# Kernel tuning notes

Measured on AMD Instinct MI355X. Metric: run time of the kernel, lower is better.

The kernel has to match this reference:

```python
import jax, jax.numpy as jnp
import numpy as np

N, E, H, C, NG = 50000, 800000, 4, 64, 32
HC = H * C  # 256


def setup_inputs() -> dict:
    key = jax.random.key(0)
    ks = jax.random.split(key, 32)
    f32 = jnp.float32
    def rn(k, shape, s=0.1):
        return jax.random.normal(k, shape, dtype=f32) * s
    inp = {}
    inp['x'] = jax.random.normal(ks[0], (N, 4), dtype=f32)
    inp['edge_index'] = jax.random.randint(ks[1], (2, E), 0, N, dtype=jnp.int32)
    inp['edge_attr'] = jax.random.normal(ks[2], (E, 1), dtype=f32)
    inp['batch'] = jnp.sort(jax.random.randint(ks[3], (N,), 0, NG, dtype=jnp.int32))
    # encoder
    inp['enc_w'] = rn(ks[4], (4, 64)); inp['enc_b'] = rn(ks[5], (64,))
    # GATv2 layer 1: in 64 -> H*C (lin_l source, lin_r target, lin_edge, att, bias)
    inp['g1_wl'] = rn(ks[6], (64, HC)); inp['g1_bl'] = rn(ks[7], (HC,))
    inp['g1_wr'] = rn(ks[8], (64, HC)); inp['g1_br'] = rn(ks[9], (HC,))
    inp['g1_we'] = rn(ks[10], (1, HC))
    inp['g1_att'] = rn(ks[11], (H, C))
    inp['g1_bias'] = rn(ks[12], (HC,))
    # GATv2 layer 2: in 256 -> H*C
    inp['g2_wl'] = rn(ks[13], (HC, HC)); inp['g2_bl'] = rn(ks[14], (HC,))
    inp['g2_wr'] = rn(ks[15], (HC, HC)); inp['g2_br'] = rn(ks[16], (HC,))
    inp['g2_we'] = rn(ks[17], (1, HC))
    inp['g2_att'] = rn(ks[18], (H, C))
    inp['g2_bias'] = rn(ks[19], (HC,))
    # post MLP: 256 -> 128 (LayerNorm, ReLU) -> 64 (ReLU)
    inp['p1_w'] = rn(ks[20], (HC, 128)); inp['p1_b'] = rn(ks[21], (128,))
    inp['ln_g'] = jnp.ones((128,), dtype=f32); inp['ln_b'] = jnp.zeros((128,), dtype=f32)
    inp['p2_w'] = rn(ks[22], (128, 64)); inp['p2_b'] = rn(ks[23], (64,))
    return inp


def _gatv2_layer(x, src, dst, eattr, wl, bl, wr, br, we, att, bias):
    # PyG GATv2Conv: alpha_e = att . leaky_relu(lin_l(x_src) + lin_r(x_dst) + lin_edge(e))
    n = x.shape[0]
    xl = (x @ wl + bl).reshape(n, H, C)   # source-side messages
    xr = (x @ wr + br).reshape(n, H, C)   # target-side
    e = (eattr @ we).reshape(-1, H, C)
    m = jax.nn.leaky_relu(xl[src] + xr[dst] + e, 0.2)        # [E',H,C]
    alpha = jnp.einsum('ehc,hc->eh', m, att)                  # [E',H]
    amax = jax.lax.stop_gradient(jax.ops.segment_max(alpha, dst, num_segments=n))
    ex = jnp.exp(alpha - amax[dst])
    den = jax.ops.segment_sum(ex, dst, num_segments=n)
    a = ex / den[dst]                                          # softmax per dst node
    out = jax.ops.segment_sum(a[:, :, None] * xl[src], dst, num_segments=n)
    return out.reshape(n, HC) + bias


def reference(x, edge_index, edge_attr, batch, enc_w, enc_b,
              g1_wl, g1_bl, g1_wr, g1_br, g1_we, g1_att, g1_bias,
              g2_wl, g2_bl, g2_wr, g2_br, g2_we, g2_att, g2_bias,
              p1_w, p1_b, ln_g, ln_b, p2_w, p2_b):
    n = x.shape[0]
    src0, dst0 = edge_index[0], edge_index[1]
    # PyG default add_self_loops=True with fill_value='mean' for edge_attr
    deg = jnp.maximum(jax.ops.segment_sum(jnp.ones_like(edge_attr[:, 0]), dst0, num_segments=n), 1.0)
    loop_attr = jax.ops.segment_sum(edge_attr, dst0, num_segments=n) / deg[:, None]
    idx = jnp.arange(n, dtype=src0.dtype)
    src = jnp.concatenate([src0, idx]); dst = jnp.concatenate([dst0, idx])
    eattr = jnp.concatenate([edge_attr, loop_attr], axis=0)
    h = jax.nn.relu(x @ enc_w + enc_b)
    h = jax.nn.relu(_gatv2_layer(h, src, dst, eattr, g1_wl, g1_bl, g1_wr, g1_br, g1_we, g1_att, g1_bias))
    h = jax.nn.relu(_gatv2_layer(h, src, dst, eattr, g2_wl, g2_bl, g2_wr, g2_br, g2_we, g2_att, g2_bias))
    # global mean pool over graphs
    cnt = jnp.maximum(jax.ops.segment_sum(jnp.ones((n,), h.dtype), batch, num_segments=NG), 1.0)
    g = jax.ops.segment_sum(h, batch, num_segments=NG) / cnt[:, None]
    # post MLP (dropout is identity in eval)
    z = g @ p1_w + p1_b
    mu = jnp.mean(z, axis=-1, keepdims=True)
    var = jnp.mean((z - mu) ** 2, axis=-1, keepdims=True)
    z = (z - mu) / jnp.sqrt(var + 1e-5) * ln_g + ln_b
    z = jax.nn.relu(z)
    z = jax.nn.relu(z @ p2_w + p2_b)
    return z
```

## Files before the change

kernel.cpp:

```cpp
#include <hip/hip_runtime.h>

#define CDIV(a,b) (((a)+(b)-1)/(b))

typedef __bf16 bf16_t;
typedef bf16_t bf16x8 __attribute__((ext_vector_type(8)));
typedef bf16_t bf16x4 __attribute__((ext_vector_type(4)));
typedef float floatx4 __attribute__((ext_vector_type(4)));
typedef float floatx2 __attribute__((ext_vector_type(2)));

__device__ __forceinline__ int sigma2(int p) {
    int tile = p >> 7, hh = (p >> 6) & 1, m = (p >> 2) & 15, c = p & 3;
    return tile * 128 + (hh * 4 + c) * 16 + m;
}

__device__ __forceinline__ floatx2 up2(unsigned v) {
    floatx2 r;
    r.x = __uint_as_float(v << 16);
    r.y = __uint_as_float(v & 0xffff0000u);
    return r;
}

__global__ void k_deg(const int* __restrict__ ei, const float* __restrict__ ea,
                      int* __restrict__ deg, float* __restrict__ lsum, int E) {
    int e = blockIdx.x * 256 + threadIdx.x;
    if (e >= E) return;
    int d = ei[E + e];
    atomicAdd(&deg[d], 1);
    atomicAdd(&lsum[d], ea[e]);
}

__global__ void k_scanA(const int* __restrict__ deg, int* __restrict__ part, int n) {
    __shared__ int sh[256];
    int t = threadIdx.x;
    int i = blockIdx.x * 256 + t;
    int v = (i < n) ? deg[i] + 1 : 0;
    sh[t] = v;
    __syncthreads();
    for (int d = 128; d > 0; d >>= 1) { if (t < d) sh[t] += sh[t + d]; __syncthreads(); }
    if (t == 0) part[blockIdx.x] = sh[0];
}
__global__ void k_scanB(int* __restrict__ part, int nb) {
    __shared__ int sh[256];
    int t = threadIdx.x;
    int v = (t < nb) ? part[t] : 0;
    sh[t] = v;
    __syncthreads();
    for (int d = 1; d < 256; d <<= 1) {
        int u = (t >= d) ? sh[t - d] : 0;
        __syncthreads();
        sh[t] += u;
        __syncthreads();
    }
    if (t < nb) part[t] = sh[t] - v;
}
__global__ void k_scanC(const int* __restrict__ deg, const int* __restrict__ part,
                        int* __restrict__ off, float* __restrict__ lsum, int n) {
    __shared__ int sh[256];
    int t = threadIdx.x;
    int i = blockIdx.x * 256 + t;
    int dv = (i < n) ? deg[i] : 0;
    int v = (i < n) ? dv + 1 : 0;
    sh[t] = v;
    __syncthreads();
    for (int d = 1; d < 256; d <<= 1) {
        int u = (t >= d) ? sh[t - d] : 0;
        __syncthreads();
        sh[t] += u;
        __syncthreads();
    }
    int excl = part[blockIdx.x] + sh[t] - v;
    if (i < n) {
        off[i] = excl;
        lsum[i] = lsum[i] / fmaxf((float)dv, 1.0f);
    }
    if (i == n - 1) off[n] = excl + v;
}

__global__ void k_fill(const int* __restrict__ ei, const float* __restrict__ ea,
                       const float* __restrict__ lattr, const int* __restrict__ off,
                       int* __restrict__ cursor, int2* __restrict__ csr, int E, int n) {
    int e = blockIdx.x * 256 + threadIdx.x;
    int EE = E + n;
    if (e >= EE) return;
    int s, d; float a;
    if (e < E) { s = ei[e]; d = ei[E + e]; a = ea[e]; }
    else       { s = e - E; d = s;         a = lattr[s]; }
    int pos = off[d] + atomicAdd(&cursor[d], 1);
    csr[pos] = make_int2(s, __float_as_int(a));
}

__global__ void k_wcast2(const float* __restrict__ Wl, const float* __restrict__ Wr,
                         const float* __restrict__ bl, const float* __restrict__ br,
                         bf16_t* __restrict__ Wt, float* __restrict__ bias2,
                         int K, int kshift, int permK,
                         const float* __restrict__ we, const float* __restrict__ att,
                         const float* __restrict__ cb,
                         float* __restrict__ wep, float* __restrict__ attp,
                         float* __restrict__ cbp) {
    int idx = blockIdx.x * 256 + threadIdx.x;
    if (idx < 512) bias2[idx] = (idx < 256) ? bl[idx] : br[idx - 256];
    if (idx < 256) {
        int sg = sigma2(idx);
        wep[idx] = we[sg]; attp[idx] = att[sg]; cbp[idx] = cb[sg];
    }
    if (idx >= 512 * K) return;
    int nn = idx >> kshift, k = idx & (K - 1);
    int ks = permK ? sigma2(k) : k;
    float v = (nn < 256) ? Wl[ks * 256 + nn] : Wr[ks * 256 + (nn - 256)];
    Wt[idx] = (bf16_t)v;
}

__global__ __launch_bounds__(256) void k_gemm1_fused(
        const float* __restrict__ x, const float* __restrict__ encw,
        const float* __restrict__ encb, const bf16_t* __restrict__ Wt,
        const float* __restrict__ bias2, bf16_t* __restrict__ XL,
        bf16_t* __restrict__ XR, int nrows) {
    __shared__ bf16_t As[128 * 32];
    __shared__ bf16_t Bs[128 * 32];
    int tid = threadIdx.x;
    int w = tid >> 6, lane = tid & 63;
    int quad = lane >> 4, m = lane & 15;
    int row0 = blockIdx.x * 128;
    bf16x8 afr[2][2];
    floatx4 acc[2][8];

    for (int ctile = 0; ctile < 4; ++ctile) {
        int n0 = ctile * 128;
#pragma unroll
        for (int rt = 0; rt < 2; ++rt)
#pragma unroll
            for (int ct = 0; ct < 8; ++ct)
                acc[rt][ct] = (floatx4){0.f, 0.f, 0.f, 0.f};
        for (int k0c = 0; k0c < 2; ++k0c) {
            __syncthreads();
            if (ctile == 0) {
#pragma unroll
                for (int i = 0; i < 2; ++i) {
                    int c = tid + i * 256;
                    int r = c >> 2, kc = c & 3;
                    int sw = (kc + (r >> 1)) & 3;
                    int gr = row0 + r; if (gr >= nrows) gr = nrows - 1;
                    float4 xv = ((const float4*)x)[gr];
                    bf16x8 v;
#pragma unroll
                    for (int kk = 0; kk < 8; ++kk) {
                        int k = k0c * 32 + kc * 8 + kk;
                        float s = encb[k];
                        s = fmaf(xv.x, encw[k], s);
                        s = fmaf(xv.y, encw[64 + k], s);
                        s = fmaf(xv.z, encw[128 + k], s);
                        s = fmaf(xv.w, encw[192 + k], s);
                        v[kk] = (bf16_t)fmaxf(s, 0.0f);
                    }
                    *(bf16x8*)&As[r * 32 + sw * 8] = v;
                }
            }
#pragma unroll
            for (int i = 0; i < 2; ++i) {
                int c = tid + i * 256;
                int r = c >> 2, kc = c & 3;
                int sw = (kc + (r >> 1)) & 3;
                bf16x8 v = *(const bf16x8*)&Wt[(size_t)(n0 + r) * 64 + k0c * 32 + kc * 8];
                *(bf16x8*)&Bs[r * 32 + sw * 8] = v;
            }
            __syncthreads();
            if (ctile == 0) {
#pragma unroll
                for (int rt = 0; rt < 2; ++rt) {
                    int ar = w * 32 + rt * 16 + m;
                    afr[k0c][rt] = *(bf16x8*)&As[ar * 32 + (((quad + (ar >> 1)) & 3) * 8)];
                }
            }
            bf16x8 bfr[8];
#pragma unroll
            for (int ct = 0; ct < 8; ++ct) {
                int br = ct * 16 + m;
                bfr[ct] = *(bf16x8*)&Bs[br * 32 + (((quad + (br >> 1)) & 3) * 8)];
            }
#pragma unroll
            for (int ct = 0; ct < 8; ++ct) {
                acc[0][ct] = __builtin_amdgcn_mfma_f32_16x16x32_bf16(afr[k0c][0], bfr[ct], acc[0][ct], 0, 0, 0);
                acc[1][ct] = __builtin_amdgcn_mfma_f32_16x16x32_bf16(afr[k0c][1], bfr[ct], acc[1][ct], 0, 0, 0);
            }
        }
        int tile = ctile & 1;
        bf16_t* dst = (ctile < 2) ? XL : XR;
        float bv[8];
#pragma unroll
        for (int ct = 0; ct < 8; ++ct) bv[ct] = bias2[n0 + ct * 16 + m];
#pragma unroll
        for (int rt = 0; rt < 2; ++rt) {
#pragma unroll
            for (int i = 0; i < 4; ++i) {
                int row = row0 + w * 32 + rt * 16 + quad * 4 + i;
                if (row < nrows) {
                    bf16x4 v0, v1;
#pragma unroll
                    for (int ct = 0; ct < 4; ++ct) {
                        v0[ct] = (bf16_t)(acc[rt][ct][i] + bv[ct]);
                        v1[ct] = (bf16_t)(acc[rt][ct + 4][i] + bv[ct + 4]);
                    }
                    *(bf16x4*)&dst[(size_t)row * 256 + tile * 128 + m * 4] = v0;
                    *(bf16x4*)&dst[(size_t)row * 256 + tile * 128 + 64 + m * 4] = v1;
                }
            }
        }
    }
}

__global__ __launch_bounds__(256) void k_gemm2(
        const bf16_t* __restrict__ Hb, const bf16_t* __restrict__ Wt,
        const float* __restrict__ bias2, bf16_t* __restrict__ XL,
        bf16_t* __restrict__ XR, int nrows) {
    const int K = 256;
    __shared__ bf16_t As[128 * 32];
    __shared__ bf16_t Bs[128 * 32];
    int tid = threadIdx.x;
    int w = tid >> 6, lane = tid & 63;
    int quad = lane >> 4, m = lane & 15;
    int row0 = blockIdx.x * 128;
    bf16x8 afr[8][2];
    floatx4 acc[2][8];

    for (int ctile = 0; ctile < 4; ++ctile) {
        int n0 = ctile * 128;
#pragma unroll
        for (int rt = 0; rt < 2; ++rt)
#pragma unroll
            for (int ct = 0; ct < 8; ++ct)
                acc[rt][ct] = (floatx4){0.f, 0.f, 0.f, 0.f};
        for (int k0c = 0; k0c < 8; ++k0c) {
            __syncthreads();
            if (ctile == 0) {
#pragma unroll
                for (int i = 0; i < 2; ++i) {
                    int c = tid + i * 256;
                    int r = c >> 2, kc = c & 3;
                    int sw = (kc + (r >> 1)) & 3;
                    int gr = row0 + r; if (gr >= nrows) gr = nrows - 1;
                    bf16x8 v = *(const bf16x8*)&Hb[(size_t)gr * K + k0c * 32 + kc * 8];
                    *(bf16x8*)&As[r * 32 + sw * 8] = v;
                }
            }
#pragma unroll
            for (int i = 0; i < 2; ++i) {
                int c = tid + i * 256;
                int r = c >> 2, kc = c & 3;
                int sw = (kc + (r >> 1)) & 3;
                bf16x8 v = *(const bf16x8*)&Wt[(size_t)(n0 + r) * K + k0c * 32 + kc * 8];
                *(bf16x8*)&Bs[r * 32 + sw * 8] = v;
            }
            __syncthreads();
            if (ctile == 0) {
#pragma unroll
                for (int rt = 0; rt < 2; ++rt) {
                    int ar = w * 32 + rt * 16 + m;
                    afr[k0c][rt] = *(bf16x8*)&As[ar * 32 + (((quad + (ar >> 1)) & 3) * 8)];
                }
            }
            bf16x8 bfr[8];
#pragma unroll
            for (int ct = 0; ct < 8; ++ct) {
                int br = ct * 16 + m;
                bfr[ct] = *(bf16x8*)&Bs[br * 32 + (((quad + (br >> 1)) & 3) * 8)];
            }
#pragma unroll
            for (int ct = 0; ct < 8; ++ct) {
                acc[0][ct] = __builtin_amdgcn_mfma_f32_16x16x32_bf16(afr[k0c][0], bfr[ct], acc[0][ct], 0, 0, 0);
                acc[1][ct] = __builtin_amdgcn_mfma_f32_16x16x32_bf16(afr[k0c][1], bfr[ct], acc[1][ct], 0, 0, 0);
            }
        }
        int tile = ctile & 1;
        bf16_t* dst = (ctile < 2) ? XL : XR;
        float bv[8];
#pragma unroll
        for (int ct = 0; ct < 8; ++ct) bv[ct] = bias2[n0 + ct * 16 + m];
#pragma unroll
        for (int rt = 0; rt < 2; ++rt) {
#pragma unroll
            for (int i = 0; i < 4; ++i) {
                int row = row0 + w * 32 + rt * 16 + quad * 4 + i;
                if (row < nrows) {
                    bf16x4 v0, v1;
#pragma unroll
                    for (int ct = 0; ct < 4; ++ct) {
                        v0[ct] = (bf16_t)(acc[rt][ct][i] + bv[ct]);
                        v1[ct] = (bf16_t)(acc[rt][ct + 4][i] + bv[ct + 4]);
                    }
                    *(bf16x4*)&dst[(size_t)row * 256 + tile * 128 + m * 4] = v0;
                    *(bf16x4*)&dst[(size_t)row * 256 + tile * 128 + 64 + m * 4] = v1;
                }
            }
        }
    }
}

__device__ __forceinline__ void pair_step(
        int p, int p1, int half, int loff,
        const int2* __restrict__ csr, const bf16_t* __restrict__ XL,
        floatx2 xr01, floatx2 xr23, floatx2 xr45, floatx2 xr67,
        floatx2 wv01, floatx2 wv23, floatx2 wv45, floatx2 wv67,
        floatx2 av01, floatx2 av23, floatx2 av45, floatx2 av67,
        float& s, floatx2& a01, floatx2& a23, floatx2& a45, floatx2& a67) {
    int idx = p + half;
    bool valid = idx < p1;
    int idc = valid ? idx : p1 - 1;
    int2 ed = csr[idc];
    int src = ed.x;
    float eav = __int_as_float(ed.y);
    uint4 u = *(const uint4*)((const char*)XL + (size_t)src * 512 + loff);
    floatx2 x01 = up2(u.x), x23 = up2(u.y), x45 = up2(u.z), x67 = up2(u.w);
    floatx2 t01 = x01 + xr01 + eav * wv01;
    floatx2 t23 = x23 + xr23 + eav * wv23;
    floatx2 t45 = x45 + xr45 + eav * wv45;
    floatx2 t67 = x67 + xr67 + eav * wv67;
    t01 = __builtin_elementwise_max(t01, 0.2f * t01);
    t23 = __builtin_elementwise_max(t23, 0.2f * t23);
    t45 = __builtin_elementwise_max(t45, 0.2f * t45);
    t67 = __builtin_elementwise_max(t67, 0.2f * t67);
    floatx2 d = t01 * av01 + t23 * av23 + t45 * av45 + t67 * av67;
    float al = d.x + d.y;
    al += __shfl_xor(al, 1);
    al += __shfl_xor(al, 2);
    al += __shfl_xor(al, 4);
    float wg = valid ? exp2f(al) : 0.0f;
    s += wg;
    a01 += wg * x01; a23 += wg * x23; a45 += wg * x45; a67 += wg * x67;
}

__global__ void k_conv(
                       const bf16_t* __restrict__ XL, const bf16_t* __restrict__ XR,
                       const float* __restrict__ wep, const float* __restrict__ attp,
                       const int2* __restrict__ csr,
                       const int* __restrict__ off, const float* __restrict__ cbp,
                       bf16_t* __restrict__ outb, int n) {
    int wid = (blockIdx.x * 256 + threadIdx.x) >> 6;
    int lane = threadIdx.x & 63;
    if (wid >= n) return;
    int l = lane & 31, half = lane >> 5;
    int loff = l * 16;
    uint4 ur = *(const uint4*)((const char*)XR + (size_t)wid * 512 + loff);
    floatx2 xr01 = up2(ur.x), xr23 = up2(ur.y), xr45 = up2(ur.z), xr67 = up2(ur.w);
    float4 wa = ((const float4*)wep)[2 * l], wb = ((const float4*)wep)[2 * l + 1];
    float4 aa = ((const float4*)attp)[2 * l], ab = ((const float4*)attp)[2 * l + 1];
    floatx2 wv01 = {wa.x, wa.y}, wv23 = {wa.z, wa.w};
    floatx2 wv45 = {wb.x, wb.y}, wv67 = {wb.z, wb.w};
    const float LOG2E = 1.44269504f;
    floatx2 av01 = {aa.x * LOG2E, aa.y * LOG2E}, av23 = {aa.z * LOG2E, aa.w * LOG2E};
    floatx2 av45 = {ab.x * LOG2E, ab.y * LOG2E}, av67 = {ab.z * LOG2E, ab.w * LOG2E};
    int p0 = off[wid], p1 = off[wid + 1];
    float s = 0.f;
    floatx2 a01 = {0.f, 0.f}, a23 = {0.f, 0.f}, a45 = {0.f, 0.f}, a67 = {0.f, 0.f};
    int p = p0;
    for (; p + 4 <= p1; p += 4) {
        pair_step(p,     p1, half, loff, csr, XL, xr01, xr23, xr45, xr67,
                  wv01, wv23, wv45, wv67, av01, av23, av45, av67, s, a01, a23, a45, a67);
        pair_step(p + 2, p1, half, loff, csr, XL, xr01, xr23, xr45, xr67,
                  wv01, wv23, wv45, wv67, av01, av23, av45, av67, s, a01, a23, a45, a67);
    }
    for (; p < p1; p += 2)
        pair_step(p,     p1, half, loff, csr, XL, xr01, xr23, xr45, xr67,
                  wv01, wv23, wv45, wv67, av01, av23, av45, av67, s, a01, a23, a45, a67);
    s += __shfl_xor(s, 32);
    a01.x += __shfl_xor(a01.x, 32); a01.y += __shfl_xor(a01.y, 32);
    a23.x += __shfl_xor(a23.x, 32); a23.y += __shfl_xor(a23.y, 32);
    a45.x += __shfl_xor(a45.x, 32); a45.y += __shfl_xor(a45.y, 32);
    a67.x += __shfl_xor(a67.x, 32); a67.y += __shfl_xor(a67.y, 32);
    if (half == 0) {
        float inv = 1.0f / s;
        float4 ba = ((const float4*)cbp)[2 * l], bb = ((const float4*)cbp)[2 * l + 1];
        bf16x8 ob;
        ob[0] = (bf16_t)fmaxf(fmaf(a01.x, inv, ba.x), 0.f);
        ob[1] = (bf16_t)fmaxf(fmaf(a01.y, inv, ba.y), 0.f);
        ob[2] = (bf16_t)fmaxf(fmaf(a23.x, inv, ba.z), 0.f);
        ob[3] = (bf16_t)fmaxf(fmaf(a23.y, inv, ba.w), 0.f);
        ob[4] = (bf16_t)fmaxf(fmaf(a45.x, inv, bb.x), 0.f);
        ob[5] = (bf16_t)fmaxf(fmaf(a45.y, inv, bb.y), 0.f);
        ob[6] = (bf16_t)fmaxf(fmaf(a67.x, inv, bb.z), 0.f);
        ob[7] = (bf16_t)fmaxf(fmaf(a67.y, inv, bb.w), 0.f);
        *(bf16x8*)&outb[(size_t)wid * 256 + l * 8] = ob;
    }
}

__global__ void k_pool(const bf16_t* __restrict__ h, const int* __restrict__ batch,
                       float* __restrict__ gsum, float* __restrict__ gcnt, int n) {
    int j = threadIdx.x;
    int start = blockIdx.x * 32;
    if (start >= n) return;
    int end = start + 32; if (end > n) end = n;
    int cur = batch[start];
    float acc = 0.0f, cnt = 0.0f;
    for (int i = start; i < end; ++i) {
        int g = batch[i];
        if (g != cur) {
            atomicAdd(&gsum[cur * 256 + j], acc);
            if (j == 0) atomicAdd(&gcnt[cur], cnt);
            acc = 0.0f; cnt = 0.0f; cur = g;
        }
        acc += (float)h[(size_t)i * 256 + j];
        cnt += 1.0f;
    }
    atomicAdd(&gsum[cur * 256 + j], acc);
    if (j == 0) atomicAdd(&gcnt[cur], cnt);
}

__global__ void k_mlp(const float* __restrict__ gsum, const float* __restrict__ gcnt,
                      const float* __restrict__ p1w, const float* __restrict__ p1b,
                      const float* __restrict__ lng, const float* __restrict__ lnb,
                      const float* __restrict__ p2w, const float* __restrict__ p2b,
                      float* __restrict__ out) {
    int g = blockIdx.x;
    int t = threadIdx.x;
    __shared__ float gv[256];
    __shared__ float z[128];
    __shared__ float red[128];
    float invc = 1.0f / fmaxf(gcnt[g], 1.0f);
    gv[sigma2(t)]       = gsum[g * 256 + t] * invc;
    gv[sigma2(t + 128)] = gsum[g * 256 + 128 + t] * invc;
    __syncthreads();
    float z1 = p1b[t];
    for (int k = 0; k < 256; ++k) z1 = fmaf(gv[k], p1w[k * 128 + t], z1);
    red[t] = z1;
    __syncthreads();
    for (int d = 64; d > 0; d >>= 1) { if (t < d) red[t] += red[t + d]; __syncthreads(); }
    float mu = red[0] * (1.0f / 128.0f);
    __syncthreads();
    float dz = z1 - mu;
    red[t] = dz * dz;
    __syncthreads();
    for (int d = 64; d > 0; d >>= 1) { if (t < d) red[t] += red[t + d]; __syncthreads(); }
    float var = red[0] * (1.0f / 128.0f);
    float zn = dz * rsqrtf(var + 1e-5f) * lng[t] + lnb[t];
    z[t] = fmaxf(zn, 0.0f);
    __syncthreads();
    if (t < 64) {
        float o = p2b[t];
        for (int k = 0; k < 128; ++k) o = fmaf(z[k], p2w[k * 64 + t], o);
        out[g * 64 + t] = fmaxf(o, 0.0f);
    }
}

extern "C" void kernel_launch(void* const* d_in, const int* in_sizes, int n_in,
                              void* d_out, int out_size, void* d_ws, size_t ws_size,
                              hipStream_t stream) {
    const float* x      = (const float*)d_in[0];
    const int*   ei     = (const int*)d_in[1];
    const float* ea     = (const float*)d_in[2];
    const int*   batch  = (const int*)d_in[3];
    const float* enc_w  = (const float*)d_in[4];
    const float* enc_b  = (const float*)d_in[5];
    const float* g1_wl  = (const float*)d_in[6];
    const float* g1_bl  = (const float*)d_in[7];
    const float* g1_wr  = (const float*)d_in[8];
    const float* g1_br  = (const float*)d_in[9];
    const float* g1_we  = (const float*)d_in[10];
    const float* g1_att = (const float*)d_in[11];
    const float* g1_bias= (const float*)d_in[12];
    const float* g2_wl  = (const float*)d_in[13];
    const float* g2_bl  = (const float*)d_in[14];
    const float* g2_wr  = (const float*)d_in[15];
    const float* g2_br  = (const float*)d_in[16];
    const float* g2_we  = (const float*)d_in[17];
    const float* g2_att = (const float*)d_in[18];
    const float* g2_bias= (const float*)d_in[19];
    const float* p1_w   = (const float*)d_in[20];
    const float* p1_b   = (const float*)d_in[21];
    const float* ln_g   = (const float*)d_in[22];
    const float* ln_b   = (const float*)d_in[23];
    const float* p2_w   = (const float*)d_in[24];
    const float* p2_b   = (const float*)d_in[25];
    float* out = (float*)d_out;

    const int N  = in_sizes[3];
    const int E  = in_sizes[1] / 2;
    const int EE = E + N;
    const int NB = CDIV(N, 256);

    bf16_t* XL  = (bf16_t*)d_ws;
    bf16_t* XR  = XL + (size_t)N * 256;
    bf16_t* Hb  = XR + (size_t)N * 256;
    bf16_t* Wt  = Hb + (size_t)N * 256;
    int2*  csr  = (int2*)(Wt + 512 * 256);
    float* lsum  = (float*)(csr + EE);
    float* gsum  = lsum + N;
    float* gcnt  = gsum + 32 * 256;
    int*   deg   = (int*)(gcnt + 32);
    int*   cursor= deg + N;
    float* bias2 = (float*)(cursor + N);
    float* wep   = bias2 + 512;
    float* attp  = wep + 256;
    float* cbp   = attp + 256;
    int*   part  = (int*)(cbp + 256);
    int*   off   = part + 256;

    hipMemsetAsync(lsum, 0, (size_t)(3 * N + 32 * 256 + 32) * sizeof(float), stream);

    k_deg<<<CDIV(E, 256), 256, 0, stream>>>(ei, ea, deg, lsum, E);
    k_scanA<<<NB, 256, 0, stream>>>(deg, part, N);
    k_scanB<<<1, 256, 0, stream>>>(part, NB);
    k_scanC<<<NB, 256, 0, stream>>>(deg, part, off, lsum, N);
    k_fill<<<CDIV(EE, 256), 256, 0, stream>>>(ei, ea, lsum, off, cursor, csr, E, N);

    k_wcast2<<<CDIV(512 * 64, 256), 256, 0, stream>>>(g1_wl, g1_wr, g1_bl, g1_br, Wt, bias2,
                                                      64, 6, 0, g1_we, g1_att, g1_bias,
                                                      wep, attp, cbp);
    k_gemm1_fused<<<CDIV(N, 128), 256, 0, stream>>>(x, enc_w, enc_b, Wt, bias2, XL, XR, N);
    k_conv<<<CDIV(N, 4), 256, 0, stream>>>(XL, XR, wep, attp, csr, off, cbp, Hb, N);

    k_wcast2<<<CDIV(512 * 256, 256), 256, 0, stream>>>(g2_wl, g2_wr, g2_bl, g2_br, Wt, bias2,
                                                       256, 8, 1, g2_we, g2_att, g2_bias,
                                                       wep, attp, cbp);
    k_gemm2<<<CDIV(N, 128), 256, 0, stream>>>(Hb, Wt, bias2, XL, XR, N);
    k_conv<<<CDIV(N, 4), 256, 0, stream>>>(XL, XR, wep, attp, csr, off, cbp, Hb, N);

    k_pool<<<CDIV(N, 32), 256, 0, stream>>>(Hb, batch, gsum, gcnt, N);
    k_mlp<<<32, 128, 0, stream>>>(gsum, gcnt, p1_w, p1_b, ln_g, ln_b, p2_w, p2_b, out);
}
```

Measured before the change: 474.5 us.

## Store XL/XR in FP8 and fuse mean-pool into second conv kernel

The GEMM epilogues now pack the source and target projections to FP8 (e4m3 via cvt_pk_fp8) instead of bf16. This halves the bytes of the random per-edge gathers in the attention/aggregation kernel, which dominate memory traffic. Separately, the second conv kernel gets a POOL template variant that reduces each block's four node rows in shared memory and atomically adds them into the per-graph sums, removing the k_pool kernel and the write and re-read of the layer-2 output. The cost is much lower precision on intermediate activations, which risks numerical tolerance, plus many more global atomics on the 32 graph rows.

```diff
diff --git a/kernel.cpp b/kernel.cpp
--- a/kernel.cpp
+++ b/kernel.cpp
@@ -3,6 +3,7 @@
 #define CDIV(a,b) (((a)+(b)-1)/(b))
 
 typedef __bf16 bf16_t;
+typedef unsigned char u8;
 typedef bf16_t bf16x8 __attribute__((ext_vector_type(8)));
 typedef bf16_t bf16x4 __attribute__((ext_vector_type(4)));
 typedef float floatx4 __attribute__((ext_vector_type(4)));
@@ -13,11 +14,10 @@
     return tile * 128 + (hh * 4 + c) * 16 + m;
 }
 
-__device__ __forceinline__ floatx2 up2(unsigned v) {
-    floatx2 r;
-    r.x = __uint_as_float(v << 16);
-    r.y = __uint_as_float(v & 0xffff0000u);
-    return r;
+__device__ __forceinline__ unsigned pack4_fp8(float a, float b, float c, float d) {
+    int v = __builtin_amdgcn_cvt_pk_fp8_f32(a, b, 0, false);
+    v = __builtin_amdgcn_cvt_pk_fp8_f32(c, d, v, true);
+    return (unsigned)v;
 }
 
 __global__ void k_deg(const int* __restrict__ ei, const float* __restrict__ ea,
@@ -113,8 +113,8 @@
 __global__ __launch_bounds__(256) void k_gemm1_fused(
         const float* __restrict__ x, const float* __restrict__ encw,
         const float* __restrict__ encb, const bf16_t* __restrict__ Wt,
-        const float* __restrict__ bias2, bf16_t* __restrict__ XL,
-        bf16_t* __restrict__ XR, int nrows) {
+        const float* __restrict__ bias2, u8* __restrict__ XL,
+        u8* __restrict__ XR, int nrows) {
     __shared__ bf16_t As[128 * 32];
     __shared__ bf16_t Bs[128 * 32];
     int tid = threadIdx.x;
@@ -184,7 +184,7 @@
             }
         }
         int tile = ctile & 1;
-        bf16_t* dst = (ctile < 2) ? XL : XR;
+        u8* dst = (ctile < 2) ? XL : XR;
         float bv[8];
 #pragma unroll
         for (int ct = 0; ct < 8; ++ct) bv[ct] = bias2[n0 + ct * 16 + m];
@@ -194,14 +194,12 @@
             for (int i = 0; i < 4; ++i) {
                 int row = row0 + w * 32 + rt * 16 + quad * 4 + i;
                 if (row < nrows) {
-                    bf16x4 v0, v1;
-#pragma unroll
-                    for (int ct = 0; ct < 4; ++ct) {
-                        v0[ct] = (bf16_t)(acc[rt][ct][i] + bv[ct]);
-                        v1[ct] = (bf16_t)(acc[rt][ct + 4][i] + bv[ct + 4]);
-                    }
-                    *(bf16x4*)&dst[(size_t)row * 256 + tile * 128 + m * 4] = v0;
-                    *(bf16x4*)&dst[(size_t)row * 256 + tile * 128 + 64 + m * 4] = v1;
+                    unsigned w0 = pack4_fp8(acc[rt][0][i] + bv[0], acc[rt][1][i] + bv[1],
+                                            acc[rt][2][i] + bv[2], acc[rt][3][i] + bv[3]);
+                    unsigned w1 = pack4_fp8(acc[rt][4][i] + bv[4], acc[rt][5][i] + bv[5],
+                                            acc[rt][6][i] + bv[6], acc[rt][7][i] + bv[7]);
+                    *(unsigned*)&dst[(size_t)row * 256 + tile * 128 + m * 4] = w0;
+                    *(unsigned*)&dst[(size_t)row * 256 + tile * 128 + 64 + m * 4] = w1;
                 }
             }
         }
@@ -210,8 +208,8 @@
 
 __global__ __launch_bounds__(256) void k_gemm2(
         const bf16_t* __restrict__ Hb, const bf16_t* __restrict__ Wt,
-        const float* __restrict__ bias2, bf16_t* __restrict__ XL,
-        bf16_t* __restrict__ XR, int nrows) {
+        const float* __restrict__ bias2, u8* __restrict__ XL,
+        u8* __restrict__ XR, int nrows) {
     const int K = 256;
     __shared__ bf16_t As[128 * 32];
     __shared__ bf16_t Bs[128 * 32];
@@ -271,7 +269,7 @@
             }
         }
         int tile = ctile & 1;
-        bf16_t* dst = (ctile < 2) ? XL : XR;
+        u8* dst = (ctile < 2) ? XL : XR;
         float bv[8];
 #pragma unroll
         for (int ct = 0; ct < 8; ++ct) bv[ct] = bias2[n0 + ct * 16 + m];
@@ -281,14 +279,12 @@
             for (int i = 0; i < 4; ++i) {
                 int row = row0 + w * 32 + rt * 16 + quad * 4 + i;
                 if (row < nrows) {
-                    bf16x4 v0, v1;
-#pragma unroll
-                    for (int ct = 0; ct < 4; ++ct) {
-                        v0[ct] = (bf16_t)(acc[rt][ct][i] + bv[ct]);
-                        v1[ct] = (bf16_t)(acc[rt][ct + 4][i] + bv[ct + 4]);
-                    }
-                    *(bf16x4*)&dst[(size_t)row * 256 + tile * 128 + m * 4] = v0;
-                    *(bf16x4*)&dst[(size_t)row * 256 + tile * 128 + 64 + m * 4] = v1;
+                    unsigned w0 = pack4_fp8(acc[rt][0][i] + bv[0], acc[rt][1][i] + bv[1],
+                                            acc[rt][2][i] + bv[2], acc[rt][3][i] + bv[3]);
+                    unsigned w1 = pack4_fp8(acc[rt][4][i] + bv[4], acc[rt][5][i] + bv[5],
+                                            acc[rt][6][i] + bv[6], acc[rt][7][i] + bv[7]);
+                    *(unsigned*)&dst[(size_t)row * 256 + tile * 128 + m * 4] = w0;
+                    *(unsigned*)&dst[(size_t)row * 256 + tile * 128 + 64 + m * 4] = w1;
                 }
             }
         }
@@ -297,7 +293,7 @@
 
 __device__ __forceinline__ void pair_step(
         int p, int p1, int half, int loff,
-        const int2* __restrict__ csr, const bf16_t* __restrict__ XL,
+        const int2* __restrict__ csr, const u8* __restrict__ XL,
         floatx2 xr01, floatx2 xr23, floatx2 xr45, floatx2 xr67,
         floatx2 wv01, floatx2 wv23, floatx2 wv45, floatx2 wv67,
         floatx2 av01, floatx2 av23, floatx2 av45, floatx2 av67,
@@ -308,8 +304,11 @@
     int2 ed = csr[idc];
     int src = ed.x;
     float eav = __int_as_float(ed.y);
-    uint4 u = *(const uint4*)((const char*)XL + (size_t)src * 512 + loff);
-    floatx2 x01 = up2(u.x), x23 = up2(u.y), x45 = up2(u.z), x67 = up2(u.w);
+    uint2 u = *(const uint2*)(XL + (size_t)src * 256 + loff);
+    floatx2 x01 = __builtin_amdgcn_cvt_pk_f32_fp8(u.x, false);
+    floatx2 x23 = __builtin_amdgcn_cvt_pk_f32_fp8(u.x, true);
+    floatx2 x45 = __builtin_amdgcn_cvt_pk_f32_fp8(u.y, false);
+    floatx2 x67 = __builtin_amdgcn_cvt_pk_f32_fp8(u.y, true);
     floatx2 t01 = x01 + xr01 + eav * wv01;
     floatx2 t23 = x23 + xr23 + eav * wv23;
     floatx2 t45 = x45 + xr45 + eav * wv45;
@@ -328,19 +327,29 @@
     a01 += wg * x01; a23 += wg * x23; a45 += wg * x45; a67 += wg * x67;
 }
 
+template<int POOL>
 __global__ void k_conv(
-                       const bf16_t* __restrict__ XL, const bf16_t* __restrict__ XR,
+                       const u8* __restrict__ XL, const u8* __restrict__ XR,
                        const float* __restrict__ wep, const float* __restrict__ attp,
                        const int2* __restrict__ csr,
                        const int* __restrict__ off, const float* __restrict__ cbp,
-                       bf16_t* __restrict__ outb, int n) {
+                       bf16_t* __restrict__ outb, const int* __restrict__ batch,
+                       float* __restrict__ gsum, float* __restrict__ gcnt, int n) {
+    __shared__ float psh[POOL ? 4 : 1][POOL ? 256 : 1];
+    __shared__ int pg[4];
     int wid = (blockIdx.x * 256 + threadIdx.x) >> 6;
+    int wv_id = threadIdx.x >> 6;
     int lane = threadIdx.x & 63;
-    if (wid >= n) return;
+    bool vn = wid < n;
+    if (!POOL && !vn) return;
+    int wclamp = vn ? wid : n - 1;
     int l = lane & 31, half = lane >> 5;
-    int loff = l * 16;
-    uint4 ur = *(const uint4*)((const char*)XR + (size_t)wid * 512 + loff);
-    floatx2 xr01 = up2(ur.x), xr23 = up2(ur.y), xr45 = up2(ur.z), xr67 = up2(ur.w);
+    int loff = l * 8;
+    uint2 ur = *(const uint2*)(XR + (size_t)wclamp * 256 + loff);
+    floatx2 xr01 = __builtin_amdgcn_cvt_pk_f32_fp8(ur.x, false);
+    floatx2 xr23 = __builtin_amdgcn_cvt_pk_f32_fp8(ur.x, true);
+    floatx2 xr45 = __builtin_amdgcn_cvt_pk_f32_fp8(ur.y, false);
+    floatx2 xr67 = __builtin_amdgcn_cvt_pk_f32_fp8(ur.y, true);
     float4 wa = ((const float4*)wep)[2 * l], wb = ((const float4*)wep)[2 * l + 1];
     float4 aa = ((const float4*)attp)[2 * l], ab = ((const float4*)attp)[2 * l + 1];
     floatx2 wv01 = {wa.x, wa.y}, wv23 = {wa.z, wa.w};
@@ -348,7 +357,7 @@
     const float LOG2E = 1.44269504f;
     floatx2 av01 = {aa.x * LOG2E, aa.y * LOG2E}, av23 = {aa.z * LOG2E, aa.w * LOG2E};
     floatx2 av45 = {ab.x * LOG2E, ab.y * LOG2E}, av67 = {ab.z * LOG2E, ab.w * LOG2E};
-    int p0 = off[wid], p1 = off[wid + 1];
+    int p0 = vn ? off[wid] : 0, p1 = vn ? off[wid + 1] : 0;
     float s = 0.f;
     floatx2 a01 = {0.f, 0.f}, a23 = {0.f, 0.f}, a45 = {0.f, 0.f}, a67 = {0.f, 0.f};
     int p = p0;
@@ -366,42 +375,46 @@
     a23.x += __shfl_xor(a23.x, 32); a23.y += __shfl_xor(a23.y, 32);
     a45.x += __shfl_xor(a45.x, 32); a45.y += __shfl_xor(a45.y, 32);
     a67.x += __shfl_xor(a67.x, 32); a67.y += __shfl_xor(a67.y, 32);
-    if (half == 0) {
-        float inv = 1.0f / s;
-        float4 ba = ((const float4*)cbp)[2 * l], bb = ((const float4*)cbp)[2 * l + 1];
-        bf16x8 ob;
-        ob[0] = (bf16_t)fmaxf(fmaf(a01.x, inv, ba.x), 0.f);
-        ob[1] = (bf16_t)fmaxf(fmaf(a01.y, inv, ba.y), 0.f);
-        ob[2] = (bf16_t)fmaxf(fmaf(a23.x, inv, ba.z), 0.f);
-        ob[3] = (bf16_t)fmaxf(fmaf(a23.y, inv, ba.w), 0.f);
-        ob[4] = (bf16_t)fmaxf(fmaf(a45.x, inv, bb.x), 0.f);
-        ob[5] = (bf16_t)fmaxf(fmaf(a45.y, inv, bb.y), 0.f);
-        ob[6] = (bf16_t)fmaxf(fmaf(a67.x, inv, bb.z), 0.f);
-        ob[7] = (bf16_t)fmaxf(fmaf(a67.y, inv, bb.w), 0.f);
-        *(bf16x8*)&outb[(size_t)wid * 256 + l * 8] = ob;
-    }
-}
-
-__global__ void k_pool(const bf16_t* __restrict__ h, const int* __restrict__ batch,
-                       float* __restrict__ gsum, float* __restrict__ gcnt, int n) {
-    int j = threadIdx.x;
-    int start = blockIdx.x * 32;
-    if (start >= n) return;
-    int end = start + 32; if (end > n) end = n;
-    int cur = batch[start];
-    float acc = 0.0f, cnt = 0.0f;
-    for (int i = start; i < end; ++i) {
-        int g = batch[i];
-        if (g != cur) {
-            atomicAdd(&gsum[cur * 256 + j], acc);
-            if (j == 0) atomicAdd(&gcnt[cur], cnt);
-            acc = 0.0f; cnt = 0.0f; cur = g;
-        }
-        acc += (float)h[(size_t)i * 256 + j];
-        cnt += 1.0f;
-    }
-    atomicAdd(&gsum[cur * 256 + j], acc);
-    if (j == 0) atomicAdd(&gcnt[cur], cnt);
+    float inv = 1.0f / s;
+    float4 ba = ((const float4*)cbp)[2 * l], bb = ((const float4*)cbp)[2 * l + 1];
+    float o0 = fmaxf(fmaf(a01.x, inv, ba.x), 0.f);
+    float o1 = fmaxf(fmaf(a01.y, inv, ba.y), 0.f);
+    float o2 = fmaxf(fmaf(a23.x, inv, ba.z), 0.f);
+    float o3 = fmaxf(fmaf(a23.y, inv, ba.w), 0.f);
+    float o4 = fmaxf(fmaf(a45.x, inv, bb.x), 0.f);
+    float o5 = fmaxf(fmaf(a45.y, inv, bb.y), 0.f);
+    float o6 = fmaxf(fmaf(a67.x, inv, bb.z), 0.f);
+    float o7 = fmaxf(fmaf(a67.y, inv, bb.w), 0.f);
+    if (!POOL) {
+        if (half == 0) {
+            bf16x8 ob;
+            ob[0] = (bf16_t)o0; ob[1] = (bf16_t)o1; ob[2] = (bf16_t)o2; ob[3] = (bf16_t)o3;
+            ob[4] = (bf16_t)o4; ob[5] = (bf16_t)o5; ob[6] = (bf16_t)o6; ob[7] = (bf16_t)o7;
+            *(bf16x8*)&outb[(size_t)wid * 256 + l * 8] = ob;
+        }
+    } else {
+        if (half == 0) {
+            float* row = psh[wv_id];
+            row[l * 8 + 0] = o0; row[l * 8 + 1] = o1; row[l * 8 + 2] = o2; row[l * 8 + 3] = o3;
+            row[l * 8 + 4] = o4; row[l * 8 + 5] = o5; row[l * 8 + 6] = o6; row[l * 8 + 7] = o7;
+            if (l == 0) pg[wv_id] = vn ? batch[wid] : -1;
+        }
+        __syncthreads();
+        int t = threadIdx.x;
+        if (t < 256) {
+            int g0 = pg[0];
+            float acc = 0.f;
+#pragma unroll
+            for (int ww = 0; ww < 4; ++ww) {
+                int g = pg[ww];
+                if (g < 0) continue;
+                if (g == g0) acc += psh[ww][t];
+                else atomicAdd(&gsum[g * 256 + t], psh[ww][t]);
+            }
+            if (g0 >= 0) atomicAdd(&gsum[g0 * 256 + t], acc);
+            if (t < 4 && pg[t] >= 0) atomicAdd(&gcnt[pg[t]], 1.0f);
+        }
+    }
 }
 
 __global__ void k_mlp(const float* __restrict__ gsum, const float* __restrict__ gcnt,
@@ -476,9 +489,9 @@
     const int EE = E + N;
     const int NB = CDIV(N, 256);
 
-    bf16_t* XL  = (bf16_t*)d_ws;
-    bf16_t* XR  = XL + (size_t)N * 256;
-    bf16_t* Hb  = XR + (size_t)N * 256;
+    u8*     XL  = (u8*)d_ws;
+    u8*     XR  = XL + (size_t)N * 256;
+    bf16_t* Hb  = (bf16_t*)(XR + (size_t)N * 256);
     bf16_t* Wt  = Hb + (size_t)N * 256;
     int2*  csr  = (int2*)(Wt + 512 * 256);
     float* lsum  = (float*)(csr + EE);
@@ -505,14 +518,15 @@
                                                       64, 6, 0, g1_we, g1_att, g1_bias,
                                                       wep, attp, cbp);
     k_gemm1_fused<<<CDIV(N, 128), 256, 0, stream>>>(x, enc_w, enc_b, Wt, bias2, XL, XR, N);
-    k_conv<<<CDIV(N, 4), 256, 0, stream>>>(XL, XR, wep, attp, csr, off, cbp, Hb, N);
+    k_conv<0><<<CDIV(N, 4), 256, 0, stream>>>(XL, XR, wep, attp, csr, off, cbp, Hb,
+                                              nullptr, nullptr, nullptr, N);
 
     k_wcast2<<<CDIV(512 * 256, 256), 256, 0, stream>>>(g2_wl, g2_wr, g2_bl, g2_br, Wt, bias2,
                                                        256, 8, 1, g2_we, g2_att, g2_bias,
                                                        wep, attp, cbp);
     k_gemm2<<<CDIV(N, 128), 256, 0, stream>>>(Hb, Wt, bias2, XL, XR, N);
-    k_conv<<<CDIV(N, 4), 256, 0, stream>>>(XL, XR, wep, attp, csr, off, cbp, Hb, N);
-
-    k_pool<<<CDIV(N, 32), 256, 0, stream>>>(Hb, batch, gsum, gcnt, N);
+    k_conv<1><<<CDIV(N, 4), 256, 0, stream>>>(XL, XR, wep, attp, csr, off, cbp, nullptr,
+                                              batch, gsum, gcnt, N);
+
     k_mlp<<<32, 128, 0, stream>>>(gsum, gcnt, p1_w, p1_b, ln_g, ln_b, p2_w, p2_b, out);
 }
```

Result: slower. 849.5 us (+79.0%).
